# Kernel tuning notes

Measured on AMD Instinct MI355X. Metric: run time of the kernel, lower is better.

Reference implementation:

```python
import jax, jax.numpy as jnp
import numpy as np

NEG_INF = -1.0e7


def positional_encodings(max_seq_len, hidden_size):
    pos = jnp.arange(max_seq_len, dtype=jnp.float32)[:, None]
    dim = jnp.arange(hidden_size // 2, dtype=jnp.float32)[None, :]
    args = pos / (10000.0 ** (2.0 * dim / hidden_size))  # (max_seq_len, h/2)
    pe = jnp.zeros((max_seq_len, hidden_size), dtype=jnp.float32)
    pe = pe.at[:, 0::2].set(jnp.sin(args)).at[:, 1::2].set(jnp.cos(args))
    return pe


def _attention(x_q, x_kv, Wq, bq, Wk, bk, Wv, bv, scale, causal):
    # Linear layers (torch Linear: y = x @ W^T + b; here W stored as (in, out)).
    q = x_q @ Wq + bq            # (B, Sq, H)
    k = x_kv @ Wk + bk           # (B, Sk, H)
    v = x_kv @ Wv + bv           # (B, Sk, H)
    scores = jnp.einsum('bqh,bkh->bqk', q, k) * scale  # (B, Sq, Sk)
    if causal:
        sq, sk = scores.shape[1], scores.shape[2]
        # original adds neg_inf * tril(ones, diag=-1) on (B, Sk, Sq): masked when k_idx > q_idx
        mask = (jnp.arange(sk)[None, :] > jnp.arange(sq)[:, None]).astype(scores.dtype)
        scores = scores + NEG_INF * mask
    w = jax.nn.softmax(scores, axis=-1)                # (B, Sq, Sk)
    ctx = jnp.einsum('bqk,bkh->bqh', w, v)
    return ctx, jnp.transpose(w, (0, 2, 1))            # weights returned as (B, Sk, Sq)


def setup_inputs() -> dict:
    B, S_dec, S_enc, H, V, L = 8, 512, 512, 1024, 32000, 6
    key = jax.random.key(0)
    ks = jax.random.split(key, 20)
    s = 0.02
    inp = {
        'inputs': jax.random.randint(ks[0], (B, S_dec), 0, V),
        'annotations': jax.random.normal(ks[1], (B, S_enc, H), dtype=jnp.float32),
        'hidden_init': jnp.zeros((B, H), dtype=jnp.float32),
        'embedding': jax.random.normal(ks[2], (V, H), dtype=jnp.float32) * s,
        'Wq_s': jax.random.normal(ks[3], (L, H, H), dtype=jnp.float32) * s,
        'bq_s': jnp.zeros((L, H), dtype=jnp.float32),
        'Wk_s': jax.random.normal(ks[4], (L, H, H), dtype=jnp.float32) * s,
        'bk_s': jnp.zeros((L, H), dtype=jnp.float32),
        'Wv_s': jax.random.normal(ks[5], (L, H, H), dtype=jnp.float32) * s,
        'bv_s': jnp.zeros((L, H), dtype=jnp.float32),
        'Wq_c': jax.random.normal(ks[6], (L, H, H), dtype=jnp.float32) * s,
        'bq_c': jnp.zeros((L, H), dtype=jnp.float32),
        'Wk_c': jax.random.normal(ks[7], (L, H, H), dtype=jnp.float32) * s,
        'bk_c': jnp.zeros((L, H), dtype=jnp.float32),
        'Wv_c': jax.random.normal(ks[8], (L, H, H), dtype=jnp.float32) * s,
        'bv_c': jnp.zeros((L, H), dtype=jnp.float32),
        'Wm': jax.random.normal(ks[9], (L, H, H), dtype=jnp.float32) * s,
        'bm': jnp.zeros((L, H), dtype=jnp.float32),
        'Wout': jax.random.normal(ks[10], (H, V), dtype=jnp.float32) * s,
        'bout': jnp.zeros((V,), dtype=jnp.float32),
    }
    return inp


def reference(inputs, annotations, hidden_init, embedding,
              Wq_s, bq_s, Wk_s, bk_s, Wv_s, bv_s,
              Wq_c, bq_c, Wk_c, bk_c, Wv_c, bv_c,
              Wm, bm, Wout, bout):
    B, S = inputs.shape
    L, H, _ = Wq_s.shape
    scale = 1.0 / jnp.sqrt(jnp.asarray(H, dtype=jnp.float32))
    pe = positional_encodings(1000, H)
    contexts = embedding[inputs] + pe[:S]              # (B, S, H)
    enc_ws, self_ws = [], []
    for i in range(L):
        new_ctx, sw = _attention(contexts, contexts,
                                 Wq_s[i], bq_s[i], Wk_s[i], bk_s[i], Wv_s[i], bv_s[i],
                                 scale, causal=True)
        residual = contexts + new_ctx
        new_ctx, ew = _attention(residual, annotations,
                                 Wq_c[i], bq_c[i], Wk_c[i], bk_c[i], Wv_c[i], bv_c[i],
                                 scale, causal=False)
        residual = residual + new_ctx
        mlp = jax.nn.relu(residual @ Wm[i] + bm[i])
        contexts = residual + mlp
        enc_ws.append(ew)
        self_ws.append(sw)
    output = contexts @ Wout + bout                    # (B, S, V)
    return output, (jnp.stack(enc_ws), jnp.stack(self_ws))
```

## Files before the change

kernel.cpp:

```cpp
#include <hip/hip_runtime.h>

typedef __attribute__((ext_vector_type(4))) float f4;
typedef __attribute__((ext_vector_type(8))) short s8v;
typedef __attribute__((ext_vector_type(4))) short s4v;

__device__ __forceinline__ short f2bf(float f) {
  union { float f; unsigned int u; } v; v.f = f;
  unsigned int u = v.u;
  unsigned int r = 0x7fffu + ((u >> 16) & 1u);
  return (short)((u + r) >> 16);
}

__device__ __forceinline__ void glds16(const void* g, void* l) {
  __builtin_amdgcn_global_load_lds((const __attribute__((address_space(1))) void*)g,
                                   (__attribute__((address_space(3))) void*)l, 16, 0, 0);
}

template<int BIAS, int RES, int RELU, int OF32, int OBF, int SWZ>
__global__ __launch_bounds__(256) void gemm_bt(
    const unsigned short* __restrict__ A, const unsigned short* __restrict__ Bt,
    const float* __restrict__ bias, const float* __restrict__ bias2,
    const float* __restrict__ res,
    float* __restrict__ Cf, unsigned short* __restrict__ Cb,
    int lda, int ldb, int ldc, int ldcb, int ldr, int nk,
    long sA, long sB, long sC, long sCb, long sR, long sBias) {
  __shared__ __align__(16) char smem[32768];
  int tid = threadIdx.x;
  int bx = blockIdx.x, by = blockIdx.y, bz = blockIdx.z;
  if (SWZ == 1) {
    int nx = gridDim.x;
    int nwg = nx * gridDim.y;
    int id = by * nx + bx;
    int q = nwg >> 3;
    int nid = (id & 7) * q + (id >> 3);
    bx = nid % nx; by = nid / nx;
  }
  int bm0 = by * 128, bn0 = bx * 128;
  const char* Ag = (const char*)(A + bz * sA);
  const char* Bg = (const char*)(Bt + bz * sB);
  if (BIAS) { bias += bz * sBias; if (BIAS == 3) bias2 += bz * sBias; }
  int w = tid >> 6, lane = tid & 63;
  int sr = tid >> 3;
  int skb = ((tid & 7) ^ (sr & 7)) << 4;
  size_t la2 = (size_t)lda * 2, lb2 = (size_t)ldb * 2;
  char* Al = smem + w * 1024;
  char* Bl = smem + 16384 + w * 1024;
  int wm = (w >> 1) * 64, wn = (w & 1) * 64;
  int rb = lane & 15;
  int kx = (lane & 7) << 4;
  int kb0 = (lane >> 4) << 4;
  const char* Ar = smem + (wm + rb) * 128;
  const char* Br = smem + 16384 + (wn + rb) * 128;
  f4 acc[4][4] = {};
  for (int kt = 0; kt < nk; ++kt) {
    size_t ka = (size_t)kt * 128 + skb;
    __syncthreads();
#pragma unroll
    for (int p = 0; p < 4; ++p)
      glds16(Ag + (size_t)(bm0 + p * 32 + sr) * la2 + ka, Al + p * 4096);
#pragma unroll
    for (int p = 0; p < 4; ++p)
      glds16(Bg + (size_t)(bn0 + p * 32 + sr) * lb2 + ka, Bl + p * 4096);
    __syncthreads();
#pragma unroll
    for (int ks = 0; ks < 2; ++ks) {
      int kb = (kb0 + ks * 64) ^ kx;
      s8v a[4], b[4];
#pragma unroll
      for (int i = 0; i < 4; ++i) a[i] = *(const s8v*)(Ar + i * 2048 + kb);
#pragma unroll
      for (int j = 0; j < 4; ++j) b[j] = *(const s8v*)(Br + j * 2048 + kb);
#pragma unroll
      for (int i = 0; i < 4; ++i)
#pragma unroll
        for (int j = 0; j < 4; ++j)
          acc[i][j] = __builtin_amdgcn_mfma_f32_16x16x32_bf16(b[j], a[i], acc[i][j], 0, 0, 0);
    }
  }
  float* Cfp = Cf + bz * sC;
  unsigned short* Cbp = Cb + bz * sCb;
  const float* Rp = res + bz * sR;
  float* E = (float*)smem;
#pragma unroll
  for (int c = 0; c < 2; ++c) {
    __syncthreads();
    if ((w >> 1) == c) {
#pragma unroll
      for (int i = 0; i < 4; ++i) {
        int lr = i * 16 + (lane & 15);
        int sw = (lr & 7) << 2;
#pragma unroll
        for (int j = 0; j < 4; ++j) {
          int col = wn + j * 16 + ((lane >> 4) << 2);
          *(f4*)&E[lr * 128 + (col ^ sw)] = acc[i][j];
        }
      }
    }
    __syncthreads();
#pragma unroll
    for (int p = 0; p < 8; ++p) {
      int fi = p * 256 + tid;
      int row = fi >> 5, c4 = fi & 31;
      f4 v = *(const f4*)&E[row * 128 + ((c4 ^ (row & 7)) << 2)];
      int rr = bm0 + c * 64 + row;
      int col = bn0 + c4 * 4;
      if (BIAS == 1) { v[0] += bias[col]; v[1] += bias[col+1]; v[2] += bias[col+2]; v[3] += bias[col+3]; }
      if (BIAS == 2) { float bb = bias[rr]; v[0] += bb; v[1] += bb; v[2] += bb; v[3] += bb; }
      if (BIAS == 3) {
        const float* bp = (col < 1024) ? (bias + col) : (bias2 + (col - 1024));
        v[0] += bp[0]; v[1] += bp[1]; v[2] += bp[2]; v[3] += bp[3];
      }
      if (RELU) { v[0]=fmaxf(v[0],0.f); v[1]=fmaxf(v[1],0.f); v[2]=fmaxf(v[2],0.f); v[3]=fmaxf(v[3],0.f); }
      if (RES) { f4 rv = *(const f4*)(Rp + (size_t)rr * ldr + col); v[0]+=rv[0]; v[1]+=rv[1]; v[2]+=rv[2]; v[3]+=rv[3]; }
      if (OF32) *(f4*)(Cfp + (size_t)rr * ldc + col) = v;
      if (OBF) {
        s4v o; o[0]=f2bf(v[0]); o[1]=f2bf(v[1]); o[2]=f2bf(v[2]); o[3]=f2bf(v[3]);
        *(s4v*)(Cbp + (size_t)rr * ldcb + col) = o;
      }
    }
  }
}

template<int RES, int OF32, int OBF>
__global__ __launch_bounds__(256) void gemm64(
    const unsigned short* __restrict__ A, const unsigned short* __restrict__ Bt,
    const float* __restrict__ res,
    float* __restrict__ Cf, unsigned short* __restrict__ Cb,
    int lda, int ldb, int ldc, int ldcb, int ldr, int nk,
    long sA, long sB, long sC, long sCb, long sR) {
  __shared__ __align__(16) char smem[16384];
  int tid = threadIdx.x;
  int bx = blockIdx.x, by = blockIdx.y, bz = blockIdx.z;
  int bm0 = by * 64, bn0 = bx * 64;
  const char* Ag = (const char*)(A + bz * sA);
  const char* Bg = (const char*)(Bt + bz * sB);
  int w = tid >> 6, lane = tid & 63;
  int sr = tid >> 3;
  int skb = ((tid & 7) ^ (sr & 7)) << 4;
  size_t la2 = (size_t)lda * 2, lb2 = (size_t)ldb * 2;
  char* Al = smem + w * 1024;
  char* Bl = smem + 8192 + w * 1024;
  int wm = (w >> 1) * 32, wn = (w & 1) * 32;
  int rb = lane & 15;
  int kx = (lane & 7) << 4;
  int kb0 = (lane >> 4) << 4;
  const char* Ar = smem + (wm + rb) * 128;
  const char* Br = smem + 8192 + (wn + rb) * 128;
  f4 acc[2][2] = {};
  for (int kt = 0; kt < nk; ++kt) {
    size_t ka = (size_t)kt * 128 + skb;
    __syncthreads();
#pragma unroll
    for (int p = 0; p < 2; ++p)
      glds16(Ag + (size_t)(bm0 + p * 32 + sr) * la2 + ka, Al + p * 4096);
#pragma unroll
    for (int p = 0; p < 2; ++p)
      glds16(Bg + (size_t)(bn0 + p * 32 + sr) * lb2 + ka, Bl + p * 4096);
    __syncthreads();
#pragma unroll
    for (int ks = 0; ks < 2; ++ks) {
      int kb = (kb0 + ks * 64) ^ kx;
      s8v a[2], b[2];
#pragma unroll
      for (int i = 0; i < 2; ++i) a[i] = *(const s8v*)(Ar + i * 2048 + kb);
#pragma unroll
      for (int j = 0; j < 2; ++j) b[j] = *(const s8v*)(Br + j * 2048 + kb);
#pragma unroll
      for (int i = 0; i < 2; ++i)
#pragma unroll
        for (int j = 0; j < 2; ++j)
          acc[i][j] = __builtin_amdgcn_mfma_f32_16x16x32_bf16(b[j], a[i], acc[i][j], 0, 0, 0);
    }
  }
  float* Cfp = Cf + bz * sC;
  unsigned short* Cbp = Cb + bz * sCb;
  const float* Rp = res + bz * sR;
  float* E = (float*)smem;
  __syncthreads();
#pragma unroll
  for (int i = 0; i < 2; ++i) {
    int lr = wm + i * 16 + (lane & 15);
    int sw = (lr & 7) << 2;
#pragma unroll
    for (int j = 0; j < 2; ++j) {
      int col = wn + j * 16 + ((lane >> 4) << 2);
      *(f4*)&E[lr * 64 + (col ^ sw)] = acc[i][j];
    }
  }
  __syncthreads();
#pragma unroll
  for (int p = 0; p < 4; ++p) {
    int fi = p * 256 + tid;
    int row = fi >> 4, c4 = fi & 15;
    f4 v = *(const f4*)&E[row * 64 + ((c4 ^ (row & 7)) << 2)];
    int rr = bm0 + row;
    int col = bn0 + c4 * 4;
    if (RES) { f4 rv = *(const f4*)(Rp + (size_t)rr * ldr + col); v[0]+=rv[0]; v[1]+=rv[1]; v[2]+=rv[2]; v[3]+=rv[3]; }
    if (OF32) *(f4*)(Cfp + (size_t)rr * ldc + col) = v;
    if (OBF) {
      s4v o; o[0]=f2bf(v[0]); o[1]=f2bf(v[1]); o[2]=f2bf(v[2]); o[3]=f2bf(v[3]);
      *(s4v*)(Cbp + (size_t)rr * ldcb + col) = o;
    }
  }
}

__global__ __launch_bounds__(512) void gemm_logits(
    const unsigned short* __restrict__ A, const unsigned short* __restrict__ Bt,
    const float* __restrict__ bias, float* __restrict__ C) {
  __shared__ __align__(1024) char lds[147456];
  const int ldc = 32000, nk = 16;
  int tid = threadIdx.x;
  int w = tid >> 6, lane = tid & 63;
  int id = blockIdx.y * 250 + blockIdx.x;
  int nid = (id & 7) * 500 + (id >> 3);
  int bx = nid % 250, by = nid / 250;
  int bm0 = by * 256, bn0 = bx * 128;
  const size_t ld2 = 2048;
  const char* Ag = (const char*)A;
  const char* Bg = (const char*)Bt;
  int srow = (w << 3) + (lane >> 3);
  size_t ska = (size_t)(((lane & 7) ^ (lane >> 3)) << 4);
  char* bf0 = lds;
  char* bf1 = lds + 49152;
  char* bf2 = lds + 98304;
  int wm = (w >> 1) * 64;
  int wn = (w & 1) * 64;
  int rsel = lane & 15;
  int kx = (lane & 7) << 4;
  int kb0 = (lane >> 4) << 4;
  f4 acc[4][4] = {};

  auto stageH = [&](char* buf, int kt, int h) {
    size_t ka = (size_t)kt * 128 + ska;
    if (h == 0) {
      glds16(Ag + (size_t)(bm0 + srow) * ld2 + ka,       buf + w * 1024);
      glds16(Ag + (size_t)(bm0 + 64 + srow) * ld2 + ka,  buf + 8192 + w * 1024);
      glds16(Bg + (size_t)(bn0 + srow) * ld2 + ka,       buf + 32768 + w * 1024);
    } else {
      glds16(Ag + (size_t)(bm0 + 128 + srow) * ld2 + ka, buf + 16384 + w * 1024);
      glds16(Ag + (size_t)(bm0 + 192 + srow) * ld2 + ka, buf + 24576 + w * 1024);
      glds16(Bg + (size_t)(bn0 + 64 + srow) * ld2 + ka,  buf + 40960 + w * 1024);
    }
  };
  auto phase = [&](const char* buf, int ks) {
    const char* Ab = buf + (wm + rsel) * 128;
    const char* Bb = buf + 32768 + (wn + rsel) * 128;
    int kb = (kb0 + ks * 64) ^ kx;
    s8v a0 = *(const s8v*)(Ab + kb);
    s8v a1 = *(const s8v*)(Ab + 2048 + kb);
    s8v a2 = *(const s8v*)(Ab + 4096 + kb);
    s8v a3 = *(const s8v*)(Ab + 6144 + kb);
    s8v q0 = *(const s8v*)(Bb + kb);
    s8v q1 = *(const s8v*)(Bb + 2048 + kb);
    s8v q2 = *(const s8v*)(Bb + 4096 + kb);
    s8v q3 = *(const s8v*)(Bb + 6144 + kb);
    __builtin_amdgcn_s_setprio(1);
    acc[0][0] = __builtin_amdgcn_mfma_f32_16x16x32_bf16(q0, a0, acc[0][0], 0, 0, 0);
    acc[0][1] = __builtin_amdgcn_mfma_f32_16x16x32_bf16(q1, a0, acc[0][1], 0, 0, 0);
    acc[0][2] = __builtin_amdgcn_mfma_f32_16x16x32_bf16(q2, a0, acc[0][2], 0, 0, 0);
    acc[0][3] = __builtin_amdgcn_mfma_f32_16x16x32_bf16(q3, a0, acc[0][3], 0, 0, 0);
    acc[1][0] = __builtin_amdgcn_mfma_f32_16x16x32_bf16(q0, a1, acc[1][0], 0, 0, 0);
    acc[1][1] = __builtin_amdgcn_mfma_f32_16x16x32_bf16(q1, a1, acc[1][1], 0, 0, 0);
    acc[1][2] = __builtin_amdgcn_mfma_f32_16x16x32_bf16(q2, a1, acc[1][2], 0, 0, 0);
    acc[1][3] = __builtin_amdgcn_mfma_f32_16x16x32_bf16(q3, a1, acc[1][3], 0, 0, 0);
    acc[2][0] = __builtin_amdgcn_mfma_f32_16x16x32_bf16(q0, a2, acc[2][0], 0, 0, 0);
    acc[2][1] = __builtin_amdgcn_mfma_f32_16x16x32_bf16(q1, a2, acc[2][1], 0, 0, 0);
    acc[2][2] = __builtin_amdgcn_mfma_f32_16x16x32_bf16(q2, a2, acc[2][2], 0, 0, 0);
    acc[2][3] = __builtin_amdgcn_mfma_f32_16x16x32_bf16(q3, a2, acc[2][3], 0, 0, 0);
    acc[3][0] = __builtin_amdgcn_mfma_f32_16x16x32_bf16(q0, a3, acc[3][0], 0, 0, 0);
    acc[3][1] = __builtin_amdgcn_mfma_f32_16x16x32_bf16(q1, a3, acc[3][1], 0, 0, 0);
    acc[3][2] = __builtin_amdgcn_mfma_f32_16x16x32_bf16(q2, a3, acc[3][2], 0, 0, 0);
    acc[3][3] = __builtin_amdgcn_mfma_f32_16x16x32_bf16(q3, a3, acc[3][3], 0, 0, 0);
    __builtin_amdgcn_s_setprio(0);
  };

  stageH(bf0, 0, 0); stageH(bf0, 0, 1);
  stageH(bf1, 1, 0); stageH(bf1, 1, 1);

  for (int t = 0; t < nk - 2; ++t) {
    stageH(bf2, t + 2, 0);
    asm volatile("s_waitcnt vmcnt(9)" ::: "memory");
    __builtin_amdgcn_s_barrier();
    __builtin_amdgcn_sched_barrier(0);
    phase(bf0, 0);
    __builtin_amdgcn_s_barrier();
    stageH(bf2, t + 2, 1);
    __builtin_amdgcn_s_barrier();
    __builtin_amdgcn_sched_barrier(0);
    phase(bf0, 1);
    __builtin_amdgcn_s_barrier();
    char* tp = bf0; bf0 = bf1; bf1 = bf2; bf2 = tp;
  }
  asm volatile("s_waitcnt vmcnt(6)" ::: "memory");
  __builtin_amdgcn_s_barrier();
  __builtin_amdgcn_sched_barrier(0);
  phase(bf0, 0);
  __builtin_amdgcn_s_barrier();
  __builtin_amdgcn_sched_barrier(0);
  phase(bf0, 1);
  __builtin_amdgcn_s_barrier();
  asm volatile("s_waitcnt vmcnt(0)" ::: "memory");
  __builtin_amdgcn_s_barrier();
  __builtin_amdgcn_sched_barrier(0);
  phase(bf1, 0);
  phase(bf1, 1);

  float* E = (float*)lds;
  __syncthreads();
#pragma unroll
  for (int i = 0; i < 4; ++i) {
    int lr = wm + i * 16 + (lane & 15);
    int sw = (lr & 7) << 2;
#pragma unroll
    for (int j = 0; j < 4; ++j) {
      int col = wn + j * 16 + ((lane >> 4) << 2);
      *(f4*)&E[lr * 128 + (col ^ sw)] = acc[i][j];
    }
  }
  __syncthreads();
#pragma unroll
  for (int p = 0; p < 16; ++p) {
    int fi = p * 512 + tid;
    int row = fi >> 5, c4 = fi & 31;
    f4 v = *(const f4*)&E[row * 128 + ((c4 ^ (row & 7)) << 2)];
    int rr = bm0 + row;
    int col = bn0 + c4 * 4;
    v[0] += bias[col]; v[1] += bias[col+1]; v[2] += bias[col+2]; v[3] += bias[col+3];
    __builtin_nontemporal_store(v, (f4*)(C + (size_t)rr * ldc + col));
  }
}

__device__ __forceinline__ void wtrans_tile(const float* src, unsigned short* dst,
                                            int rows, int cols, int c0, int r0) {
  __shared__ float t[64][65];
  int tx = threadIdx.x & 63, ty = threadIdx.x >> 6;
#pragma unroll
  for (int j = 0; j < 16; ++j) {
    int r = j * 4 + ty;
    t[r][tx] = src[(size_t)(r0 + r) * cols + c0 + tx];
  }
  __syncthreads();
#pragma unroll
  for (int j = 0; j < 16; ++j) {
    int n = j * 4 + ty;
    dst[(size_t)(c0 + n) * rows + r0 + tx] = (unsigned short)f2bf(t[tx][n]);
  }
}

__global__ __launch_bounds__(256) void wtrans_k(const float* __restrict__ src,
                                                unsigned short* __restrict__ dst,
                                                int rows, int cols) {
  wtrans_tile(src, dst, rows, cols, blockIdx.x * 64, blockIdx.y * 64);
}

__global__ __launch_bounds__(256) void wtrans_all_k(
    const float* __restrict__ w0, const float* __restrict__ w1,
    const float* __restrict__ w2, const float* __restrict__ w3,
    const float* __restrict__ w4, const float* __restrict__ w5,
    const float* __restrict__ w6, unsigned short* __restrict__ dst) {
  int z = blockIdx.z;
  int l = z / 7, wi = z % 7;
  const float* src;
  switch (wi) {
    case 0: src = w0; break;
    case 1: src = w1; break;
    case 2: src = w2; break;
    case 3: src = w3; break;
    case 4: src = w4; break;
    case 5: src = w5; break;
    default: src = w6; break;
  }
  src += (size_t)l * 1024 * 1024;
  unsigned short* d = dst + (size_t)z * 1024 * 1024;
  wtrans_tile(src, d, 1024, 1024, blockIdx.x * 64, blockIdx.y * 64);
}

__global__ __launch_bounds__(256) void convbf_k(const float* __restrict__ src,
                                                unsigned short* __restrict__ dst, int n4) {
  int i = blockIdx.x * 256 + threadIdx.x;
  if (i >= n4) return;
  f4 f = ((const f4*)src)[i];
  s4v v;
  v[0] = f2bf(f[0]); v[1] = f2bf(f[1]); v[2] = f2bf(f[2]); v[3] = f2bf(f[3]);
  ((s4v*)dst)[i] = v;
}

template<int CAUSAL>
__global__ __launch_bounds__(512) void smt_k(const float* __restrict__ Sf,
                                             float* __restrict__ outT,
                                             unsigned short* __restrict__ Wb) {
  __shared__ float T[32][524];
  int b = blockIdx.y;
  int q0 = blockIdx.x * 32;
  int t = threadIdx.x;
  const float* Sp = Sf + ((size_t)b * 512 + q0) * 512;
#pragma unroll
  for (int j = 0; j < 8; ++j) {
    int idx = t + 512 * j;
    int r = idx >> 7, c4 = idx & 127;
    f4 v = *(const f4*)(Sp + (size_t)r * 512 + c4 * 4);
    *(f4*)&T[r][c4 * 4] = v;
  }
  __syncthreads();
  int w = t >> 6, l = t & 63;
  int r = 4 * w + (l >> 4);
  int l16 = l & 15;
  int q = q0 + r;
  const float scale = 0.03125f;
  float v[32];
#pragma unroll
  for (int j = 0; j < 32; ++j) {
    int k = l16 + 16 * j;
    float x = T[r][k] * scale;
    if (CAUSAL && k > q) x += -1.0e7f;
    v[j] = x;
  }
  float m = v[0];
#pragma unroll
  for (int j = 1; j < 32; ++j) m = fmaxf(m, v[j]);
  m = fmaxf(m, __shfl_xor(m, 1)); m = fmaxf(m, __shfl_xor(m, 2));
  m = fmaxf(m, __shfl_xor(m, 4)); m = fmaxf(m, __shfl_xor(m, 8));
  float s = 0.f;
#pragma unroll
  for (int j = 0; j < 32; ++j) { v[j] = __expf(v[j] - m); s += v[j]; }
  s += __shfl_xor(s, 1); s += __shfl_xor(s, 2);
  s += __shfl_xor(s, 4); s += __shfl_xor(s, 8);
  float inv = 1.0f / s;
#pragma unroll
  for (int j = 0; j < 32; ++j) T[r][l16 + 16 * j] = v[j] * inv;
  __syncthreads();
  float* op = outT + (size_t)b * 512 * 512 + q0;
  int ql = t & 31, kb = t >> 5;
#pragma unroll
  for (int i = 0; i < 32; ++i) {
    int k = kb + 16 * i;
    __builtin_nontemporal_store(T[ql][k], &op[(size_t)k * 512 + ql]);
  }
  unsigned short* wp = Wb + ((size_t)b * 512 + q0) * 512;
#pragma unroll
  for (int i = 0; i < 4; ++i) {
    int rr = 4 * w + i;
    const float* row = &T[rr][l * 8];
    s8v o;
#pragma unroll
    for (int j = 0; j < 8; ++j) o[j] = f2bf(row[j]);
    *(s8v*)(wp + (size_t)rr * 512 + l * 8) = o;
  }
}

__global__ __launch_bounds__(256) void embed_pe_k(const int* __restrict__ ids,
                                                  const float* __restrict__ emb,
                                                  float* __restrict__ ctx,
                                                  unsigned short* __restrict__ ctxb) {
  int row = blockIdx.x;
  int s = row & 511;
  int t = threadIdx.x;
  int id = ids[row];
  f4 e = *(const f4*)(emb + (size_t)id * 1024 + t * 4);
  int j0 = 2 * t, j1 = 2 * t + 1;
  float fr0 = powf(10000.0f, -2.0f * (float)j0 / 1024.0f);
  float fr1 = powf(10000.0f, -2.0f * (float)j1 / 1024.0f);
  float s0, c0, s1, c1;
  sincosf((float)s * fr0, &s0, &c0);
  sincosf((float)s * fr1, &s1, &c1);
  f4 o;
  o[0] = e[0] + s0; o[1] = e[1] + c0; o[2] = e[2] + s1; o[3] = e[3] + c1;
  *(f4*)(ctx + (size_t)row * 1024 + t * 4) = o;
  s4v ob;
  ob[0] = f2bf(o[0]); ob[1] = f2bf(o[1]); ob[2] = f2bf(o[2]); ob[3] = f2bf(o[3]);
  *(s4v*)(ctxb + (size_t)row * 1024 + t * 4) = ob;
}

extern "C" void kernel_launch(void* const* d_in, const int* in_sizes, int n_in,
                              void* d_out, int out_size, void* d_ws, size_t ws_size,
                              hipStream_t stream) {
  const int B = 8, S = 512, H = 1024, V = 32000, L = 6;
  const int M = B * S;

  const int* ids = (const int*)d_in[0];
  const float* ann = (const float*)d_in[1];
  const float* emb = (const float*)d_in[3];
  const float* bq_s = (const float*)d_in[5];
  const float* bk_s = (const float*)d_in[7];
  const float* bv_s = (const float*)d_in[9];
  const float* bq_c = (const float*)d_in[11];
  const float* bk_c = (const float*)d_in[13];
  const float* bv_c = (const float*)d_in[15];
  const float* bm = (const float*)d_in[17];
  const float* Wout = (const float*)d_in[18];
  const float* bout = (const float*)d_in[19];
  float* out = (float*)d_out;

  char* ws = (char*)d_ws;
  if (ws_size < ((size_t)164 << 20)) return;
  float* X0 = (float*)ws;
  unsigned short* Xs0 = (unsigned short*)(ws + ((size_t)16 << 20));
  unsigned short* Xs1 = (unsigned short*)(ws + ((size_t)24 << 20));
  unsigned short* QKbf = (unsigned short*)(ws + ((size_t)32 << 20));
  unsigned short* Vtbf = (unsigned short*)(ws + ((size_t)48 << 20));
  float* Sbuf = (float*)(ws + ((size_t)56 << 20));
  unsigned short* Wbf = (unsigned short*)(ws + ((size_t)64 << 20));
  unsigned short* annbf = (unsigned short*)(ws + ((size_t)68 << 20));
  unsigned short* WT = (unsigned short*)(ws + ((size_t)76 << 20));
  unsigned short* KcAll = (unsigned short*)d_out;
  unsigned short* VtcAll = (unsigned short*)((char*)d_out + ((size_t)48 << 20));

  size_t enc_off = (size_t)M * V;
  size_t self_off = enc_off + (size_t)L * B * S * S;

  long sQ = (long)S * H;
  long sS = (long)S * S;
  const size_t WSZ = (size_t)H * H;
  const long sW7 = (long)(7 * WSZ);

  embed_pe_k<<<M, 256, 0, stream>>>(ids, emb, X0, Xs0);
  convbf_k<<<(M * H / 4 + 255) / 256, 256, 0, stream>>>(ann, annbf, M * H / 4);
  wtrans_all_k<<<dim3(16, 16, 42), 256, 0, stream>>>(
      (const float*)d_in[4], (const float*)d_in[6], (const float*)d_in[8],
      (const float*)d_in[10], (const float*)d_in[12], (const float*)d_in[14],
      (const float*)d_in[16], WT);
  gemm_bt<1, 0, 0, 0, 1, 0><<<dim3(8, 32, 6), 256, 0, stream>>>(
      annbf, WT + 4 * WSZ, bk_c, nullptr, nullptr, nullptr, KcAll,
      H, H, 0, H, 0, 16, 0, sW7, 0, (long)M * H, 0, H);
  gemm_bt<2, 0, 0, 0, 1, 0><<<dim3(32, 8, 6), 256, 0, stream>>>(
      WT + 5 * WSZ, annbf, bv_c, nullptr, nullptr, nullptr, VtcAll,
      H, H, 0, M, 0, 16, sW7, 0, 0, (long)H * M, 0, H);

  unsigned short* Xa = Xs0;
  unsigned short* Xb = Xs1;

  for (int l = 0; l < L; ++l) {
    size_t bo = (size_t)l * H;
    unsigned short* WTl = WT + (size_t)l * 7 * WSZ;

    gemm_bt<3, 0, 0, 0, 1, 0><<<dim3(16, 32), 256, 0, stream>>>(
        Xa, WTl, bq_s + bo, bk_s + bo, nullptr, nullptr, QKbf,
        H, H, 0, 2048, 0, 16, 0, 0, 0, 0, 0, 0);
    gemm_bt<2, 0, 0, 0, 1, 0><<<dim3(32, 8), 256, 0, stream>>>(
        WTl + 2 * WSZ, Xa, bv_s + bo, nullptr, nullptr, nullptr, Vtbf,
        H, H, 0, M, 0, 16, 0, 0, 0, 0, 0, 0);
    gemm64<0, 1, 0><<<dim3(8, 8, B), 256, 0, stream>>>(
        QKbf, QKbf + 1024, nullptr, Sbuf, nullptr,
        2048, 2048, S, 0, 0, 16, (long)S * 2048, (long)S * 2048, sS, 0, 0);
    smt_k<1><<<dim3(16, B), 512, 0, stream>>>(
        Sbuf, out + self_off + (size_t)l * B * S * S, Wbf);
    gemm64<1, 1, 1><<<dim3(16, 8, B), 256, 0, stream>>>(
        Wbf, Vtbf, X0, X0, Xb,
        S, M, H, H, H, 8, sS, 512, sQ, sQ, sQ);
    gemm_bt<1, 0, 0, 0, 1, 0><<<dim3(8, 32), 256, 0, stream>>>(
        Xb, WTl + 3 * WSZ, bq_c + bo, nullptr, nullptr, nullptr, QKbf,
        H, H, 0, 1024, 0, 16, 0, 0, 0, 0, 0, 0);
    gemm64<0, 1, 0><<<dim3(8, 8, B), 256, 0, stream>>>(
        QKbf, KcAll + (size_t)l * M * H, nullptr, Sbuf, nullptr,
        1024, 1024, S, 0, 0, 16, (long)S * 1024, (long)S * 1024, sS, 0, 0);
    smt_k<0><<<dim3(16, B), 512, 0, stream>>>(
        Sbuf, out + enc_off + (size_t)l * B * S * S, Wbf);
    gemm64<1, 1, 1><<<dim3(16, 8, B), 256, 0, stream>>>(
        Wbf, VtcAll + (size_t)l * H * M, X0, X0, Xa,
        S, M, H, H, H, 8, sS, 512, sQ, sQ, sQ);
    gemm_bt<1, 1, 1, 1, 1, 0><<<dim3(8, 32), 256, 0, stream>>>(
        Xa, WTl + 6 * WSZ, bm + bo, nullptr, X0, X0, Xb,
        H, H, H, H, H, 16, 0, 0, 0, 0, 0, 0);
    unsigned short* tb = Xa; Xa = Xb; Xb = tb;
  }

  wtrans_k<<<dim3(V / 64, H / 64), 256, 0, stream>>>(Wout, WT, H, V);
  gemm_logits<<<dim3(250, 16), 512, 0, stream>>>(Xa, WT, bout, out);
}
```

Measured before the change: 1.631 ms.

## Triple-buffer GEMM k-loop with async LDS prefetch and priority-raised MFMA

Replaces the synchronous load-then-compute k-loop of the 128x128 bf16 GEMM with a three-buffer pipeline that prefetches tiles two steps ahead using direct-to-LDS loads, explicit vmcnt waits and raw barriers, splitting each stage's loads across the two compute phases. MFMA blocks are wrapped with s_setprio to favour math issue, and the epilogue writes the full tile in one pass using the larger LDS. The cost is 96KB of LDS per block, which reduces how many blocks can reside per CU, and more fragile hand-scheduled synchronisation.

After: 1.473 ms. 9.7% less time.

```diff
diff --git a/kernel.cpp b/kernel.cpp
--- a/kernel.cpp
+++ b/kernel.cpp
@@ -16,25 +16,17 @@
                                    (__attribute__((address_space(3))) void*)l, 16, 0, 0);
 }
 
-template<int BIAS, int RES, int RELU, int OF32, int OBF, int SWZ>
-__global__ __launch_bounds__(256) void gemm_bt(
+template<int BIAS, int RES, int RELU, int OF32, int OBF>
+__global__ __launch_bounds__(256) void gemmp(
     const unsigned short* __restrict__ A, const unsigned short* __restrict__ Bt,
     const float* __restrict__ bias, const float* __restrict__ bias2,
     const float* __restrict__ res,
     float* __restrict__ Cf, unsigned short* __restrict__ Cb,
     int lda, int ldb, int ldc, int ldcb, int ldr, int nk,
     long sA, long sB, long sC, long sCb, long sR, long sBias) {
-  __shared__ __align__(16) char smem[32768];
+  __shared__ __align__(1024) char lds[98304];
   int tid = threadIdx.x;
   int bx = blockIdx.x, by = blockIdx.y, bz = blockIdx.z;
-  if (SWZ == 1) {
-    int nx = gridDim.x;
-    int nwg = nx * gridDim.y;
-    int id = by * nx + bx;
-    int q = nwg >> 3;
-    int nid = (id & 7) * q + (id >> 3);
-    bx = nid % nx; by = nid / nx;
-  }
   int bm0 = by * 128, bn0 = bx * 128;
   const char* Ag = (const char*)(A + bz * sA);
   const char* Bg = (const char*)(Bt + bz * sB);
@@ -43,80 +35,113 @@
   int sr = tid >> 3;
   int skb = ((tid & 7) ^ (sr & 7)) << 4;
   size_t la2 = (size_t)lda * 2, lb2 = (size_t)ldb * 2;
-  char* Al = smem + w * 1024;
-  char* Bl = smem + 16384 + w * 1024;
+  char* bf0 = lds;
+  char* bf1 = lds + 32768;
+  char* bf2 = lds + 65536;
   int wm = (w >> 1) * 64, wn = (w & 1) * 64;
   int rb = lane & 15;
   int kx = (lane & 7) << 4;
   int kb0 = (lane >> 4) << 4;
-  const char* Ar = smem + (wm + rb) * 128;
-  const char* Br = smem + 16384 + (wn + rb) * 128;
   f4 acc[4][4] = {};
-  for (int kt = 0; kt < nk; ++kt) {
+
+  auto stageH = [&](char* buf, int kt, int h) {
     size_t ka = (size_t)kt * 128 + skb;
-    __syncthreads();
-#pragma unroll
-    for (int p = 0; p < 4; ++p)
-      glds16(Ag + (size_t)(bm0 + p * 32 + sr) * la2 + ka, Al + p * 4096);
-#pragma unroll
-    for (int p = 0; p < 4; ++p)
-      glds16(Bg + (size_t)(bn0 + p * 32 + sr) * lb2 + ka, Bl + p * 4096);
-    __syncthreads();
-#pragma unroll
-    for (int ks = 0; ks < 2; ++ks) {
-      int kb = (kb0 + ks * 64) ^ kx;
-      s8v a[4], b[4];
-#pragma unroll
-      for (int i = 0; i < 4; ++i) a[i] = *(const s8v*)(Ar + i * 2048 + kb);
-#pragma unroll
-      for (int j = 0; j < 4; ++j) b[j] = *(const s8v*)(Br + j * 2048 + kb);
-#pragma unroll
-      for (int i = 0; i < 4; ++i)
-#pragma unroll
-        for (int j = 0; j < 4; ++j)
-          acc[i][j] = __builtin_amdgcn_mfma_f32_16x16x32_bf16(b[j], a[i], acc[i][j], 0, 0, 0);
-    }
-  }
+    if (h == 0) {
+      glds16(Ag + (size_t)(bm0 + sr) * la2 + ka,            buf + w * 1024);
+      glds16(Ag + (size_t)(bm0 + 32 + sr) * la2 + ka,       buf + 4096 + w * 1024);
+      glds16(Bg + (size_t)(bn0 + sr) * lb2 + ka,            buf + 16384 + w * 1024);
+      glds16(Bg + (size_t)(bn0 + 32 + sr) * lb2 + ka,       buf + 20480 + w * 1024);
+    } else {
+      glds16(Ag + (size_t)(bm0 + 64 + sr) * la2 + ka,       buf + 8192 + w * 1024);
+      glds16(Ag + (size_t)(bm0 + 96 + sr) * la2 + ka,       buf + 12288 + w * 1024);
+      glds16(Bg + (size_t)(bn0 + 64 + sr) * lb2 + ka,       buf + 24576 + w * 1024);
+      glds16(Bg + (size_t)(bn0 + 96 + sr) * lb2 + ka,       buf + 28672 + w * 1024);
+    }
+  };
+  auto phase = [&](const char* buf, int ks) {
+    const char* Ar = buf + (wm + rb) * 128;
+    const char* Br = buf + 16384 + (wn + rb) * 128;
+    int kb = (kb0 + ks * 64) ^ kx;
+    s8v a[4], b[4];
+#pragma unroll
+    for (int i = 0; i < 4; ++i) a[i] = *(const s8v*)(Ar + i * 2048 + kb);
+#pragma unroll
+    for (int j = 0; j < 4; ++j) b[j] = *(const s8v*)(Br + j * 2048 + kb);
+    __builtin_amdgcn_s_setprio(1);
+#pragma unroll
+    for (int i = 0; i < 4; ++i)
+#pragma unroll
+      for (int j = 0; j < 4; ++j)
+        acc[i][j] = __builtin_amdgcn_mfma_f32_16x16x32_bf16(b[j], a[i], acc[i][j], 0, 0, 0);
+    __builtin_amdgcn_s_setprio(0);
+  };
+
+  stageH(bf0, 0, 0); stageH(bf0, 0, 1);
+  stageH(bf1, 1, 0); stageH(bf1, 1, 1);
+
+  for (int t = 0; t < nk - 2; ++t) {
+    stageH(bf2, t + 2, 0);
+    asm volatile("s_waitcnt vmcnt(12)" ::: "memory");
+    __builtin_amdgcn_s_barrier();
+    __builtin_amdgcn_sched_barrier(0);
+    phase(bf0, 0);
+    __builtin_amdgcn_s_barrier();
+    stageH(bf2, t + 2, 1);
+    __builtin_amdgcn_s_barrier();
+    __builtin_amdgcn_sched_barrier(0);
+    phase(bf0, 1);
+    __builtin_amdgcn_s_barrier();
+    char* tp = bf0; bf0 = bf1; bf1 = bf2; bf2 = tp;
+  }
+  asm volatile("s_waitcnt vmcnt(8)" ::: "memory");
+  __builtin_amdgcn_s_barrier();
+  __builtin_amdgcn_sched_barrier(0);
+  phase(bf0, 0);
+  __builtin_amdgcn_s_barrier();
+  __builtin_amdgcn_sched_barrier(0);
+  phase(bf0, 1);
+  __builtin_amdgcn_s_barrier();
+  asm volatile("s_waitcnt vmcnt(0)" ::: "memory");
+  __builtin_amdgcn_s_barrier();
+  __builtin_amdgcn_sched_barrier(0);
+  phase(bf1, 0);
+  phase(bf1, 1);
+
   float* Cfp = Cf + bz * sC;
   unsigned short* Cbp = Cb + bz * sCb;
   const float* Rp = res + bz * sR;
-  float* E = (float*)smem;
-#pragma unroll
-  for (int c = 0; c < 2; ++c) {
-    __syncthreads();
-    if ((w >> 1) == c) {
-#pragma unroll
-      for (int i = 0; i < 4; ++i) {
-        int lr = i * 16 + (lane & 15);
-        int sw = (lr & 7) << 2;
-#pragma unroll
-        for (int j = 0; j < 4; ++j) {
-          int col = wn + j * 16 + ((lane >> 4) << 2);
-          *(f4*)&E[lr * 128 + (col ^ sw)] = acc[i][j];
-        }
-      }
-    }
-    __syncthreads();
-#pragma unroll
-    for (int p = 0; p < 8; ++p) {
-      int fi = p * 256 + tid;
-      int row = fi >> 5, c4 = fi & 31;
-      f4 v = *(const f4*)&E[row * 128 + ((c4 ^ (row & 7)) << 2)];
-      int rr = bm0 + c * 64 + row;
-      int col = bn0 + c4 * 4;
-      if (BIAS == 1) { v[0] += bias[col]; v[1] += bias[col+1]; v[2] += bias[col+2]; v[3] += bias[col+3]; }
-      if (BIAS == 2) { float bb = bias[rr]; v[0] += bb; v[1] += bb; v[2] += bb; v[3] += bb; }
-      if (BIAS == 3) {
-        const float* bp = (col < 1024) ? (bias + col) : (bias2 + (col - 1024));
-        v[0] += bp[0]; v[1] += bp[1]; v[2] += bp[2]; v[3] += bp[3];
-      }
-      if (RELU) { v[0]=fmaxf(v[0],0.f); v[1]=fmaxf(v[1],0.f); v[2]=fmaxf(v[2],0.f); v[3]=fmaxf(v[3],0.f); }
-      if (RES) { f4 rv = *(const f4*)(Rp + (size_t)rr * ldr + col); v[0]+=rv[0]; v[1]+=rv[1]; v[2]+=rv[2]; v[3]+=rv[3]; }
-      if (OF32) *(f4*)(Cfp + (size_t)rr * ldc + col) = v;
-      if (OBF) {
-        s4v o; o[0]=f2bf(v[0]); o[1]=f2bf(v[1]); o[2]=f2bf(v[2]); o[3]=f2bf(v[3]);
-        *(s4v*)(Cbp + (size_t)rr * ldcb + col) = o;
-      }
+  float* E = (float*)lds;
+  __syncthreads();
+#pragma unroll
+  for (int i = 0; i < 4; ++i) {
+    int lr = wm + i * 16 + (lane & 15);
+    int sw = (lr & 7) << 2;
+#pragma unroll
+    for (int j = 0; j < 4; ++j) {
+      int col = wn + j * 16 + ((lane >> 4) << 2);
+      *(f4*)&E[lr * 128 + (col ^ sw)] = acc[i][j];
+    }
+  }
+  __syncthreads();
+#pragma unroll
+  for (int p = 0; p < 16; ++p) {
+    int fi = p * 256 + tid;
+    int row = fi >> 5, c4 = fi & 31;
+    f4 v = *(const f4*)&E[row * 128 + ((c4 ^ (row & 7)) << 2)];
+    int rr = bm0 + row;
+    int col = bn0 + c4 * 4;
+    if (BIAS == 1) { v[0] += bias[col]; v[1] += bias[col+1]; v[2] += bias[col+2]; v[3] += bias[col+3]; }
+    if (BIAS == 2) { float bb = bias[rr]; v[0] += bb; v[1] += bb; v[2] += bb; v[3] += bb; }
+    if (BIAS == 3) {
+      const float* bp = (col < 1024) ? (bias + col) : (bias2 + (col - 1024));
+      v[0] += bp[0]; v[1] += bp[1]; v[2] += bp[2]; v[3] += bp[3];
+    }
+    if (RELU) { v[0]=fmaxf(v[0],0.f); v[1]=fmaxf(v[1],0.f); v[2]=fmaxf(v[2],0.f); v[3]=fmaxf(v[3],0.f); }
+    if (RES) { f4 rv = *(const f4*)(Rp + (size_t)rr * ldr + col); v[0]+=rv[0]; v[1]+=rv[1]; v[2]+=rv[2]; v[3]+=rv[3]; }
+    if (OF32) *(f4*)(Cfp + (size_t)rr * ldc + col) = v;
+    if (OBF) {
+      s4v o; o[0]=f2bf(v[0]); o[1]=f2bf(v[1]); o[2]=f2bf(v[2]); o[3]=f2bf(v[3]);
+      *(s4v*)(Cbp + (size_t)rr * ldcb + col) = o;
     }
   }
 }
@@ -519,10 +544,10 @@
       (const float*)d_in[4], (const float*)d_in[6], (const float*)d_in[8],
       (const float*)d_in[10], (const float*)d_in[12], (const float*)d_in[14],
       (const float*)d_in[16], WT);
-  gemm_bt<1, 0, 0, 0, 1, 0><<<dim3(8, 32, 6), 256, 0, stream>>>(
+  gemmp<1, 0, 0, 0, 1><<<dim3(8, 32, 6), 256, 0, stream>>>(
       annbf, WT + 4 * WSZ, bk_c, nullptr, nullptr, nullptr, KcAll,
       H, H, 0, H, 0, 16, 0, sW7, 0, (long)M * H, 0, H);
-  gemm_bt<2, 0, 0, 0, 1, 0><<<dim3(32, 8, 6), 256, 0, stream>>>(
+  gemmp<2, 0, 0, 0, 1><<<dim3(32, 8, 6), 256, 0, stream>>>(
       WT + 5 * WSZ, annbf, bv_c, nullptr, nullptr, nullptr, VtcAll,
       H, H, 0, M, 0, 16, sW7, 0, 0, (long)H * M, 0, H);
 
@@ -533,10 +558,10 @@
     size_t bo = (size_t)l * H;
     unsigned short* WTl = WT + (size_t)l * 7 * WSZ;
 
-    gemm_bt<3, 0, 0, 0, 1, 0><<<dim3(16, 32), 256, 0, stream>>>(
+    gemmp<3, 0, 0, 0, 1><<<dim3(16, 32), 256, 0, stream>>>(
         Xa, WTl, bq_s + bo, bk_s + bo, nullptr, nullptr, QKbf,
         H, H, 0, 2048, 0, 16, 0, 0, 0, 0, 0, 0);
-    gemm_bt<2, 0, 0, 0, 1, 0><<<dim3(32, 8), 256, 0, stream>>>(
+    gemmp<2, 0, 0, 0, 1><<<dim3(32, 8), 256, 0, stream>>>(
         WTl + 2 * WSZ, Xa, bv_s + bo, nullptr, nullptr, nullptr, Vtbf,
         H, H, 0, M, 0, 16, 0, 0, 0, 0, 0, 0);
     gemm64<0, 1, 0><<<dim3(8, 8, B), 256, 0, stream>>>(
@@ -547,7 +572,7 @@
     gemm64<1, 1, 1><<<dim3(16, 8, B), 256, 0, stream>>>(
         Wbf, Vtbf, X0, X0, Xb,
         S, M, H, H, H, 8, sS, 512, sQ, sQ, sQ);
-    gemm_bt<1, 0, 0, 0, 1, 0><<<dim3(8, 32), 256, 0, stream>>>(
+    gemmp<1, 0, 0, 0, 1><<<dim3(8, 32), 256, 0, stream>>>(
         Xb, WTl + 3 * WSZ, bq_c + bo, nullptr, nullptr, nullptr, QKbf,
         H, H, 0, 1024, 0, 16, 0, 0, 0, 0, 0, 0);
     gemm64<0, 1, 0><<<dim3(8, 8, B), 256, 0, stream>>>(
@@ -558,7 +583,7 @@
     gemm64<1, 1, 1><<<dim3(16, 8, B), 256, 0, stream>>>(
         Wbf, VtcAll + (size_t)l * H * M, X0, X0, Xa,
         S, M, H, H, H, 8, sS, 512, sQ, sQ, sQ);
-    gemm_bt<1, 1, 1, 1, 1, 0><<<dim3(8, 32), 256, 0, stream>>>(
+    gemmp<1, 1, 1, 1, 1><<<dim3(8, 32), 256, 0, stream>>>(
         Xa, WTl + 6 * WSZ, bm + bo, nullptr, X0, X0, Xb,
         H, H, H, H, H, 16, 0, 0, 0, 0, 0, 0);
     unsigned short* tb = Xa; Xa = Xb; Xb = tb;
```
